# Optimization experiments

Hardware: AMD Instinct MI355X
Metric: run time of the kernel (lower is better)

Reference implementation:

```python
import jax, jax.numpy as jnp
import numpy as np
import math

B, T, D = 2, 2048, 1024
NH = 16
HD = D // NH


def setup_inputs() -> dict:
    key = jax.random.key(0)
    k1, k2, k3 = jax.random.split(key, 3)
    scale = 0.02
    x = jax.random.normal(k1, (B, T, D), dtype=jnp.float32)
    Wqkv = jax.random.normal(k2, (D, 3 * D), dtype=jnp.float32) * scale
    bqkv = jnp.zeros((3 * D,), dtype=jnp.float32)
    Wproj = jax.random.normal(k3, (D, D), dtype=jnp.float32) * scale
    bproj = jnp.zeros((D,), dtype=jnp.float32)
    return {"x": x, "Wqkv": Wqkv, "bqkv": bqkv, "Wproj": Wproj, "bproj": bproj}


def reference(x, Wqkv, bqkv, Wproj, bproj):
    b, t, c = x.shape
    qkv = x @ Wqkv + bqkv                      # [B,T,3D]
    q, k, v = jnp.split(qkv, 3, axis=2)
    # [B,T,NH,HD] -> [B,NH,T,HD]
    q = q.reshape(b, t, NH, HD).transpose(0, 2, 1, 3)
    k = k.reshape(b, t, NH, HD).transpose(0, 2, 1, 3)
    v = v.reshape(b, t, NH, HD).transpose(0, 2, 1, 3)
    att = jnp.einsum('bhqd,bhkd->bhqk', q, k) / math.sqrt(HD)  # [B,NH,T,T]
    causal = jnp.tril(jnp.ones((t, t), dtype=bool))
    att = jnp.where(causal, att, -jnp.inf)
    att = jax.nn.softmax(att, axis=-1)
    y = jnp.einsum('bhqk,bhkd->bhqd', att, v)  # [B,NH,T,HD]
    y = y.transpose(0, 2, 1, 3).reshape(b, t, c)
    return y @ Wproj + bproj
```

## Files before the change

### kernel.cpp

```cpp
#include <hip/hip_runtime.h>
#include <hip/hip_bf16.h>

#define B_   2
#define T_   2048
#define D_   1024
#define NH_  16
#define HD_  64
#define MROWS (B_*T_)
#define HEADELEMS (B_*NH_*T_*HD_)

#define QSCALE 0.180336880f

typedef unsigned short u16;
typedef unsigned int   u32;

typedef float f32x4  __attribute__((ext_vector_type(4)));
typedef short bf16x8 __attribute__((ext_vector_type(8)));

#define GLP(g, l) __builtin_amdgcn_global_load_lds(                         \
    (const __attribute__((address_space(1))) void*)(g),                     \
    (__attribute__((address_space(3))) void*)(l), 16, 0, 0)

struct Fc { static constexpr bool value = false; };
struct Tc { static constexpr bool value = true;  };

__device__ __forceinline__ u16 f2bf(float f) {
    u32 x = __float_as_uint(f);
    u32 r = (x + 0x7fffu + ((x >> 16) & 1u)) >> 16;
    return (u16)r;
}
__device__ __forceinline__ u32 pkbf2(float a, float b) {
    __hip_bfloat162 h = __float22bfloat162_rn(make_float2(a, b));
    union { __hip_bfloat162 h2; u32 u; } cv; cv.h2 = h; return cv.u;
}

__device__ __forceinline__ void transpose_tile(const float* in, u16* out,
                                               int K, int N, int bx, int by,
                                               int t, float (*Ts)[65])
{
    const int n0 = bx * 64;
    const int k0 = by * 64;
    #pragma unroll
    for (int pass = 0; pass < 4; pass++) {
        const int r = pass * 16 + (t >> 4);
        const int c = (t & 15) * 4;
        float4 v = *(const float4*)(in + (size_t)(k0 + r) * N + n0 + c);
        Ts[r][c] = v.x; Ts[r][c+1] = v.y; Ts[r][c+2] = v.z; Ts[r][c+3] = v.w;
    }
    __syncthreads();
    #pragma unroll
    for (int pass = 0; pass < 2; pass++) {
        const int nn = pass * 32 + (t >> 3);
        const int kk = (t & 7) * 8;
        u16 o[8];
        #pragma unroll
        for (int j = 0; j < 8; j++) o[j] = f2bf(Ts[kk + j][nn]);
        *(uint4*)(out + (size_t)(n0 + nn) * K + k0 + kk) = *(const uint4*)o;
    }
}

__global__ __launch_bounds__(256)
void prep_kernel(const float* __restrict__ x, const float* __restrict__ Wqkv,
                 const float* __restrict__ Wproj, u16* __restrict__ xb,
                 u16* __restrict__ WqkvT, u16* __restrict__ WprojT)
{
    __shared__ float Ts[64][65];
    const int bid = blockIdx.x;
    const int t   = threadIdx.x;
    if (bid < 4096) {
        int i = bid * 256 + t;
        float4 v = ((const float4*)x)[i];
        ushort4 o;
        o.x = f2bf(v.x); o.y = f2bf(v.y); o.z = f2bf(v.z); o.w = f2bf(v.w);
        ((ushort4*)xb)[i] = o;
    } else if (bid < 4096 + 768) {
        int tb = bid - 4096;
        transpose_tile(Wqkv, WqkvT, D_, 3*D_, tb % 48, tb / 48, t, Ts);
    } else {
        int tb = bid - 4864;
        transpose_tile(Wproj, WprojT, D_, D_, tb % 16, tb / 16, t, Ts);
    }
}

__global__ __launch_bounds__(256)
void transpose_conv_kernel(const float* __restrict__ in, u16* __restrict__ out,
                           int K, int N)
{
    __shared__ float Ts[64][65];
    transpose_tile(in, out, K, N, blockIdx.x, blockIdx.y, threadIdx.x, Ts);
}

template <int MODE>
__global__ __launch_bounds__(256)
void gemm_mfma(const u16* __restrict__ A, const u16* __restrict__ BT,
               const float* __restrict__ bias, void* __restrict__ outv,
               int M, int N, int K)
{
    __shared__ u16 As[128][32];
    __shared__ u16 Bs[128][32];

    const int t    = threadIdx.x;
    const int wave = t >> 6;
    const int lane = t & 63;
    const int l16  = lane & 15;
    const int quad = lane >> 4;

    const int m0 = blockIdx.y * 128;
    const int n0 = blockIdx.x * 128;
    const int mb = (wave >> 1) * 64;
    const int nb = (wave & 1) * 64;

    const int r0a  = wave * 16;
    const int r0b  = 64 + wave * 16;
    const int lr_a = r0a + (lane >> 2);
    const int lr_b = r0b + (lane >> 2);
    const int sega = (((lane & 3) ^ ((lr_a >> 1) & 3))) * 8;
    const int segb = (((lane & 3) ^ ((lr_b >> 1) & 3))) * 8;

    const u16* gA0 = A  + (size_t)(m0 + lr_a) * K + sega;
    const u16* gA1 = A  + (size_t)(m0 + lr_b) * K + segb;
    const u16* gB0 = BT + (size_t)(n0 + lr_a) * K + sega;
    const u16* gB1 = BT + (size_t)(n0 + lr_b) * K + segb;

    const int fragoff = (quad ^ ((l16 >> 1) & 3)) * 8;

    f32x4 acc[4][4];
    #pragma unroll
    for (int i = 0; i < 4; i++)
        #pragma unroll
        for (int j = 0; j < 4; j++) acc[i][j] = (f32x4){0,0,0,0};

    for (int k0 = 0; k0 < K; k0 += 32) {
        __syncthreads();
        GLP(gA0 + k0, &As[r0a][0]);
        GLP(gA1 + k0, &As[r0b][0]);
        GLP(gB0 + k0, &Bs[r0a][0]);
        GLP(gB1 + k0, &Bs[r0b][0]);
        __syncthreads();

        bf16x8 af[4], bfr[4];
        #pragma unroll
        for (int i = 0; i < 4; i++)
            af[i] = *(const bf16x8*)&As[mb + i*16 + l16][fragoff];
        #pragma unroll
        for (int j = 0; j < 4; j++)
            bfr[j] = *(const bf16x8*)&Bs[nb + j*16 + l16][fragoff];

        #pragma unroll
        for (int i = 0; i < 4; i++)
            #pragma unroll
            for (int j = 0; j < 4; j++)
                acc[i][j] = __builtin_amdgcn_mfma_f32_16x16x32_bf16(
                    af[i], bfr[j], acc[i][j], 0, 0, 0);
    }

    #pragma unroll
    for (int j = 0; j < 4; j++) {
        const int n = n0 + nb + j*16 + l16;
        const float bv = bias[n];
        #pragma unroll
        for (int i = 0; i < 4; i++) {
            #pragma unroll
            for (int r = 0; r < 4; r++) {
                const int m = m0 + mb + i*16 + quad*4 + r;
                float v = acc[i][j][r] + bv;
                if (MODE == 0) {
                    ((float*)outv)[(size_t)m * N + n] = v;
                } else {
                    const int b   = m >> 11;
                    const int tt  = m & 2047;
                    const int sec = n >> 10;
                    const int dd  = n & 1023;
                    const int h   = dd >> 6;
                    const int hd  = dd & 63;
                    const size_t hbase = ((size_t)(b*NH_ + h)) * T_ * HD_;
                    size_t idx;
                    if (sec == 2)
                        idx = (size_t)2 * HEADELEMS + hbase + (size_t)hd * T_ + tt;
                    else
                        idx = (size_t)sec * HEADELEMS + hbase + (size_t)tt * HD_ + hd;
                    if (sec == 0) v *= QSCALE;
                    ((u16*)outv)[idx] = f2bf(v);
                }
            }
        }
    }
}

__global__ __launch_bounds__(256)
void attn_mfma_kernel(const u16* __restrict__ Q, const u16* __restrict__ K,
                      const u16* __restrict__ VT, u16* __restrict__ y1)
{
    __shared__ u16 Ks[2][64][72];
    __shared__ u16 Vs[2][64][72];

    const int t    = threadIdx.x;
    const int wave = t >> 6;
    const int lane = t & 63;
    const int l16  = lane & 15;
    const int quad = lane >> 4;

    const int hb = blockIdx.x;
    const int yy = blockIdx.y;
    const int a  = yy & 7, g = yy >> 3;
    const int qt = (g == 0) ? 31 - a : (g == 1) ? 16 + a
                 : (g == 2) ? 15 - a : a;
    const int b  = hb >> 4;
    const int h  = hb & 15;
    const size_t base = (size_t)hb * T_ * HD_;

    const int qw0 = qt * 64 + wave * 16;

    bf16x8 qf[2];
    {
        const u16* qp = Q + base + (size_t)(qw0 + l16) * HD_ + quad * 8;
        qf[0] = *(const bf16x8*)(qp);
        qf[1] = *(const bf16x8*)(qp + 32);
    }

    bf16x8 onesf;
    #pragma unroll
    for (int i = 0; i < 8; i++) onesf[i] = (short)0x3F80;

    f32x4 o[4];
    #pragma unroll
    for (int d = 0; d < 4; d++) o[d] = (f32x4){0,0,0,0};
    f32x4 accl = (f32x4){0,0,0,0};

    const int nsteps = qt + 1;

    const int srow = t >> 3;
    const int scol = (t & 7) * 8;

    const int srcA  = l16 + ((quad & 1) << 5);
    const int srcB  = srcA + 16;
    const bool selhi = (quad >> 1) != 0;

    uint4 kr0, kr1, vr0, vr1;
    {
        const u16* kp = K + base + (size_t)srow * HD_ + scol;
        kr0 = *(const uint4*)kp;
        kr1 = *(const uint4*)(kp + 32 * HD_);
        const u16* vp = VT + base + (size_t)srow * T_ + scol;
        vr0 = *(const uint4*)vp;
        vr1 = *(const uint4*)(vp + 32 * T_);
        *(uint4*)&Ks[0][srow][scol]      = kr0;
        *(uint4*)&Ks[0][srow + 32][scol] = kr1;
        *(uint4*)&Vs[0][srow][scol]      = vr0;
        *(uint4*)&Vs[0][srow + 32][scol] = vr1;
    }
    __syncthreads();

    auto compute_tile = [&](int cur, int k0, auto mc) {
        constexpr bool MASKED = decltype(mc)::value;
        f32x4 st[4];
        #pragma unroll
        for (int j = 0; j < 4; j++) {
            bf16x8 kf0 = *(const bf16x8*)&Ks[cur][j*16 + l16][quad * 8];
            bf16x8 kf1 = *(const bf16x8*)&Ks[cur][j*16 + l16][32 + quad * 8];
            f32x4 z = {0,0,0,0};
            z = __builtin_amdgcn_mfma_f32_16x16x32_bf16(kf0, qf[0], z, 0, 0, 0);
            st[j] = __builtin_amdgcn_mfma_f32_16x16x32_bf16(kf1, qf[1], z, 0, 0, 0);
        }

        u32 p01[4], p23[4];
        const int qi = qw0 + l16;
        #pragma unroll
        for (int j = 0; j < 4; j++) {
            const int kb = k0 + j*16 + quad*4;
            float e0 = __builtin_amdgcn_exp2f(st[j][0]);
            float e1 = __builtin_amdgcn_exp2f(st[j][1]);
            float e2 = __builtin_amdgcn_exp2f(st[j][2]);
            float e3 = __builtin_amdgcn_exp2f(st[j][3]);
            if (MASKED) {
                if (kb + 0 > qi) e0 = 0.f;
                if (kb + 1 > qi) e1 = 0.f;
                if (kb + 2 > qi) e2 = 0.f;
                if (kb + 3 > qi) e3 = 0.f;
            }
            p01[j] = pkbf2(e0, e1);
            p23[j] = pkbf2(e2, e3);
        }

        bf16x8 pf[2];
        #pragma unroll
        for (int c = 0; c < 2; c++) {
            u32 t0, t1, r01, r23, r45, r67;
            t0 = (u32)__shfl((int)p01[2*c],   srcA);
            t1 = (u32)__shfl((int)p01[2*c+1], srcA);
            r01 = selhi ? t1 : t0;
            t0 = (u32)__shfl((int)p23[2*c],   srcA);
            t1 = (u32)__shfl((int)p23[2*c+1], srcA);
            r23 = selhi ? t1 : t0;
            t0 = (u32)__shfl((int)p01[2*c],   srcB);
            t1 = (u32)__shfl((int)p01[2*c+1], srcB);
            r45 = selhi ? t1 : t0;
            t0 = (u32)__shfl((int)p23[2*c],   srcB);
            t1 = (u32)__shfl((int)p23[2*c+1], srcB);
            r67 = selhi ? t1 : t0;
            union { u32 u[4]; bf16x8 v; } pk;
            pk.u[0] = r01; pk.u[1] = r23; pk.u[2] = r45; pk.u[3] = r67;
            pf[c] = pk.v;
        }
        accl = __builtin_amdgcn_mfma_f32_16x16x32_bf16(pf[0], onesf, accl, 0, 0, 0);
        accl = __builtin_amdgcn_mfma_f32_16x16x32_bf16(pf[1], onesf, accl, 0, 0, 0);
        #pragma unroll
        for (int d = 0; d < 4; d++) {
            bf16x8 v0 = *(const bf16x8*)&Vs[cur][d*16 + l16][quad * 8];
            bf16x8 v1 = *(const bf16x8*)&Vs[cur][d*16 + l16][32 + quad * 8];
            o[d] = __builtin_amdgcn_mfma_f32_16x16x32_bf16(pf[0], v0, o[d], 0, 0, 0);
            o[d] = __builtin_amdgcn_mfma_f32_16x16x32_bf16(pf[1], v1, o[d], 0, 0, 0);
        }
    };

    for (int kt = 0; kt < nsteps; kt++) {
        const int cur = kt & 1;
        const int k0  = kt * 64;
        const bool have_next = (kt + 1 < nsteps);

        if (have_next) {
            const u16* kp = K + base + (size_t)(k0 + 64 + srow) * HD_ + scol;
            kr0 = *(const uint4*)kp;
            kr1 = *(const uint4*)(kp + 32 * HD_);
            const u16* vp = VT + base + (size_t)srow * T_ + k0 + 64 + scol;
            vr0 = *(const uint4*)vp;
            vr1 = *(const uint4*)(vp + 32 * T_);
        }

        if (kt < qt) compute_tile(cur, k0, Fc{});
        else         compute_tile(cur, k0, Tc{});

        if (have_next) {
            const int nxt = cur ^ 1;
            *(uint4*)&Ks[nxt][srow][scol]      = kr0;
            *(uint4*)&Ks[nxt][srow + 32][scol] = kr1;
            *(uint4*)&Vs[nxt][srow][scol]      = vr0;
            *(uint4*)&Vs[nxt][srow + 32][scol] = vr1;
            __syncthreads();
        }
    }

    #pragma unroll
    for (int r = 0; r < 4; r++) {
        const float inv = 1.f / accl[r];
        const int qi = qw0 + quad*4 + r;
        u16* yp = y1 + ((size_t)(b * T_ + qi)) * D_ + h * HD_ + l16;
        yp[0]  = f2bf(o[0][r] * inv);
        yp[16] = f2bf(o[1][r] * inv);
        yp[32] = f2bf(o[2][r] * inv);
        yp[48] = f2bf(o[3][r] * inv);
    }
}

extern "C" void kernel_launch(void* const* d_in, const int* in_sizes, int n_in,
                              void* d_out, int out_size, void* d_ws, size_t ws_size,
                              hipStream_t stream)
{
    const float* x     = (const float*)d_in[0];
    const float* Wqkv  = (const float*)d_in[1];
    const float* bqkv  = (const float*)d_in[2];
    const float* Wproj = (const float*)d_in[3];
    const float* bproj = (const float*)d_in[4];

    u16* scratch = (u16*)d_out;
    u16* xb      = scratch;
    u16* WqkvT   = scratch + (size_t)MROWS * D_;

    const size_t Y1E = (size_t)MROWS * D_;
    const size_t WPE = (size_t)D_ * D_;

    u16* qkv = (u16*)d_ws;
    u16* Qp  = qkv;
    u16* Kp  = qkv + (size_t)HEADELEMS;
    u16* Vtp = qkv + (size_t)2 * HEADELEMS;

    const bool huge = ws_size >= ((size_t)3 * HEADELEMS + Y1E + WPE) * 2;
    const bool big  = ws_size >= ((size_t)3 * HEADELEMS + Y1E) * 2;

    u16* y1b    = big ? qkv + (size_t)3 * HEADELEMS : scratch;
    u16* y1g    = big ? y1b : Vtp;
    u16* WprojT = huge ? qkv + (size_t)3 * HEADELEMS + Y1E : Kp;

    prep_kernel<<<huge ? 5120 : 4864, 256, 0, stream>>>(
        x, Wqkv, Wproj, xb, WqkvT, WprojT);

    gemm_mfma<1><<<dim3(3*D_/128, MROWS/128), 256, 0, stream>>>(
        xb, WqkvT, bqkv, (void*)qkv, MROWS, 3*D_, D_);

    attn_mfma_kernel<<<dim3(NH_*B_, T_/64), 256, 0, stream>>>(Qp, Kp, Vtp, y1b);

    if (!huge)
        transpose_conv_kernel<<<dim3(D_/64, D_/64), 256, 0, stream>>>(
            Wproj, WprojT, D_, D_);

    if (!big)
        (void)hipMemcpyAsync(y1g, y1b, Y1E * sizeof(u16),
                             hipMemcpyDeviceToDevice, stream);

    gemm_mfma<0><<<dim3(D_/128, MROWS/128), 256, 0, stream>>>(
        y1g, WprojT, bproj, d_out, MROWS, D_, D_);
}
```

Baseline: 195.1 us.

## Double-buffer GEMM LDS tiles and specialize QKV scatter epilogue per section

Switches the GEMM main loop to two LDS buffers, so the global-to-LDS loads for the next K tile are issued before the MFMAs on the current tile. This overlaps load latency with compute and leaves one barrier per iteration instead of two. The QKV epilogue now computes the section, batch and head indices once per block rather than per element. V-transposed outputs are written as packed 4-element 8-byte stores. The cost is double the LDS use and possible occupancy pressure, and correctness relies on global_load_lds completing before the single barrier.

```diff
diff --git a/kernel.cpp b/kernel.cpp
--- a/kernel.cpp
+++ b/kernel.cpp
@@ -96,8 +96,8 @@
                const float* __restrict__ bias, void* __restrict__ outv,
                int M, int N, int K)
 {
-    __shared__ u16 As[128][32];
-    __shared__ u16 Bs[128][32];
+    __shared__ u16 As[2][128][32];
+    __shared__ u16 Bs[2][128][32];
 
     const int t    = threadIdx.x;
     const int wave = t >> 6;
@@ -130,21 +130,31 @@
         #pragma unroll
         for (int j = 0; j < 4; j++) acc[i][j] = (f32x4){0,0,0,0};
 
-    for (int k0 = 0; k0 < K; k0 += 32) {
-        __syncthreads();
-        GLP(gA0 + k0, &As[r0a][0]);
-        GLP(gA1 + k0, &As[r0b][0]);
-        GLP(gB0 + k0, &Bs[r0a][0]);
-        GLP(gB1 + k0, &Bs[r0b][0]);
-        __syncthreads();
+    GLP(gA0, &As[0][r0a][0]);
+    GLP(gA1, &As[0][r0b][0]);
+    GLP(gB0, &Bs[0][r0a][0]);
+    GLP(gB1, &Bs[0][r0b][0]);
+    __syncthreads();
+
+    const int nk = K >> 5;
+    for (int kt = 0; kt < nk; ++kt) {
+        const int cur = kt & 1;
+        if (kt + 1 < nk) {
+            const int nxt = cur ^ 1;
+            const int kn  = (kt + 1) << 5;
+            GLP(gA0 + kn, &As[nxt][r0a][0]);
+            GLP(gA1 + kn, &As[nxt][r0b][0]);
+            GLP(gB0 + kn, &Bs[nxt][r0a][0]);
+            GLP(gB1 + kn, &Bs[nxt][r0b][0]);
+        }
 
         bf16x8 af[4], bfr[4];
         #pragma unroll
         for (int i = 0; i < 4; i++)
-            af[i] = *(const bf16x8*)&As[mb + i*16 + l16][fragoff];
+            af[i] = *(const bf16x8*)&As[cur][mb + i*16 + l16][fragoff];
         #pragma unroll
         for (int j = 0; j < 4; j++)
-            bfr[j] = *(const bf16x8*)&Bs[nb + j*16 + l16][fragoff];
+            bfr[j] = *(const bf16x8*)&Bs[cur][nb + j*16 + l16][fragoff];
 
         #pragma unroll
         for (int i = 0; i < 4; i++)
@@ -152,35 +162,65 @@
             for (int j = 0; j < 4; j++)
                 acc[i][j] = __builtin_amdgcn_mfma_f32_16x16x32_bf16(
                     af[i], bfr[j], acc[i][j], 0, 0, 0);
-    }
-
-    #pragma unroll
-    for (int j = 0; j < 4; j++) {
-        const int n = n0 + nb + j*16 + l16;
-        const float bv = bias[n];
-        #pragma unroll
-        for (int i = 0; i < 4; i++) {
+
+        __syncthreads();
+    }
+
+    if (MODE == 0) {
+        #pragma unroll
+        for (int j = 0; j < 4; j++) {
+            const int n = n0 + nb + j*16 + l16;
+            const float bv = bias[n];
             #pragma unroll
-            for (int r = 0; r < 4; r++) {
-                const int m = m0 + mb + i*16 + quad*4 + r;
-                float v = acc[i][j][r] + bv;
-                if (MODE == 0) {
-                    ((float*)outv)[(size_t)m * N + n] = v;
-                } else {
-                    const int b   = m >> 11;
-                    const int tt  = m & 2047;
-                    const int sec = n >> 10;
-                    const int dd  = n & 1023;
-                    const int h   = dd >> 6;
-                    const int hd  = dd & 63;
-                    const size_t hbase = ((size_t)(b*NH_ + h)) * T_ * HD_;
-                    size_t idx;
-                    if (sec == 2)
-                        idx = (size_t)2 * HEADELEMS + hbase + (size_t)hd * T_ + tt;
-                    else
-                        idx = (size_t)sec * HEADELEMS + hbase + (size_t)tt * HD_ + hd;
-                    if (sec == 0) v *= QSCALE;
-                    ((u16*)outv)[idx] = f2bf(v);
+            for (int i = 0; i < 4; i++) {
+                #pragma unroll
+                for (int r = 0; r < 4; r++) {
+                    const int m = m0 + mb + i*16 + quad*4 + r;
+                    ((float*)outv)[(size_t)m * N + n] = acc[i][j][r] + bv;
+                }
+            }
+        }
+    } else {
+        const int sec = n0 >> 10;
+        const int b   = m0 >> 11;
+        const int tb  = m0 & 2047;
+        if (sec < 2) {
+            const float qs = (sec == 0) ? QSCALE : 1.f;
+            #pragma unroll
+            for (int j = 0; j < 4; j++) {
+                const int n  = n0 + nb + j*16 + l16;
+                const float bv = bias[n];
+                const int dd = n & 1023;
+                const int h  = dd >> 6;
+                const int hd = dd & 63;
+                u16* op = (u16*)outv + (size_t)sec * HEADELEMS
+                        + ((size_t)(b*NH_ + h)) * T_ * HD_ + hd;
+                #pragma unroll
+                for (int i = 0; i < 4; i++) {
+                    #pragma unroll
+                    for (int r = 0; r < 4; r++) {
+                        const int tt = tb + mb + i*16 + quad*4 + r;
+                        op[(size_t)tt * HD_] = f2bf((acc[i][j][r] + bv) * qs);
+                    }
+                }
+            }
+        } else {
+            #pragma unroll
+            for (int j = 0; j < 4; j++) {
+                const int n  = n0 + nb + j*16 + l16;
+                const float bv = bias[n];
+                const int dd = n & 1023;
+                const int h  = dd >> 6;
+                const int hd = dd & 63;
+                u16* vp = (u16*)outv + (size_t)2 * HEADELEMS
+                        + ((size_t)(b*NH_ + h)) * T_ * HD_
+                        + (size_t)hd * T_ + tb + mb;
+                #pragma unroll
+                for (int i = 0; i < 4; i++) {
+                    u16 o[4];
+                    #pragma unroll
+                    for (int r = 0; r < 4; r++) o[r] = f2bf(acc[i][j][r] + bv);
+                    *(uint2*)(vp + i*16 + quad*4) = *(const uint2*)o;
                 }
             }
         }
```

Result: slower. 200.2 us (+2.6%).
